# Performance work log

Hardware: AMD Instinct MI355X
Metric: run time of the kernel (lower is better)

## Reference

```python
import jax, jax.numpy as jnp
import numpy as np

L, B, D = 64, 2048, 512

def setup_inputs() -> dict:
    key = jax.random.key(0)
    ks = jax.random.split(key, 8)
    x = jax.random.normal(ks[0], (L, B, D), dtype=jnp.float32)
    # learned parameters (torch inits them to ones; random here for a nontrivial test)
    weight_x = 1.0 + 0.1 * jax.random.normal(ks[1], (L, D), dtype=jnp.float32)
    weight_g = 1.0 + 0.1 * jax.random.normal(ks[2], (L, D), dtype=jnp.float32)
    weight_h = 1.0 + 0.1 * jax.random.normal(ks[3], (L, D), dtype=jnp.float32)
    weight_u = 1.0 + 0.1 * jax.random.normal(ks[4], (L, D), dtype=jnp.float32)
    mask = jax.random.uniform(ks[5], (L, D), dtype=jnp.float32)
    fc_w = jax.random.normal(ks[6], (1, D), dtype=jnp.float32) / np.sqrt(D)
    fc_b = jax.random.normal(ks[7], (1,), dtype=jnp.float32) / np.sqrt(D)
    return {"x": x, "weight_x": weight_x, "weight_g": weight_g,
            "weight_h": weight_h, "weight_u": weight_u, "mask": mask,
            "fc_w": fc_w, "fc_b": fc_b}

def reference(x, weight_x, weight_g, weight_h, weight_u, mask, fc_w, fc_b):
    # x: [L, B, D]; per-step weights broadcast [D] over [B, D]
    xb0 = x[0]                               # x_bar[0] = x[0]
    h0 = jnp.tanh(x[0] * weight_x[0])        # h[0]
    xb1 = h0 * weight_g[0] + x[0]            # x_bar[1]

    def step(carry, inputs):
        h_prev, xbar_t = carry
        x_t, wx, wg, wh, wu, m = inputs
        x_trans = x_t * m + xbar_t * (1.0 - m)
        u = jnp.tanh(x_trans * wx)
        f = jax.nn.sigmoid(h_prev * wh + u * wu) * m
        h_t = f * h_prev + jnp.minimum(1.0 - f, u)
        h_t = h0 + jax.nn.relu(h_t - h0)
        xbar_next = h_t * wg + x_trans
        return (h_t, xbar_next), xbar_t

    _, xb_seq = jax.lax.scan(
        step, (h0, xb1),
        (x[1:], weight_x[1:], weight_g[1:], weight_h[1:], weight_u[1:], mask[1:]))
    # x_bar = [x_bar[0], x_bar[1], ..., x_bar[L-1]]  (x_bar[L] is never written in torch)
    x_bar = jnp.concatenate([xb0[None], xb_seq], axis=0)  # [L, B, D]
    pred = jax.nn.sigmoid(jnp.einsum('lbd,od->lbo', x_bar, fc_w) + fc_b)  # [L, B, 1]
    return pred
```

## Files before the change

### kernel.cpp

```cpp
#include <hip/hip_runtime.h>

typedef float f4 __attribute__((ext_vector_type(4)));
typedef float f2 __attribute__((ext_vector_type(2)));

#define LL 64
#define BB 2048
#define DD 512
#define GB 2
#define NBLK (BB / GB)
#define DEPTH 4

__device__ __forceinline__ float fexp2(float x){ return __builtin_amdgcn_exp2f(x); }
__device__ __forceinline__ float frcpf_(float x){ return __builtin_amdgcn_rcpf(x); }
__device__ __forceinline__ float fsigm(float z){ return frcpf_(1.0f + fexp2(-1.442695040888963f*z)); }
__device__ __forceinline__ float ftanh_(float z){ return 1.0f - 2.0f*frcpf_(1.0f + fexp2(2.885390081777927f*z)); }

__device__ __forceinline__ f4 ld4(const float* __restrict__ p){
  return *(const f4*)p;
}
__device__ __forceinline__ f4 vexp2(f4 v){
  f4 r; r[0]=fexp2(v[0]); r[1]=fexp2(v[1]); r[2]=fexp2(v[2]); r[3]=fexp2(v[3]); return r;
}
__device__ __forceinline__ f4 vrcp(f4 v){
  f4 r; r[0]=frcpf_(v[0]); r[1]=frcpf_(v[1]); r[2]=frcpf_(v[2]); r[3]=frcpf_(v[3]); return r;
}

__device__ __forceinline__ float quad_reduce_dpp(float v){
  int t1 = __builtin_amdgcn_update_dpp(0, __builtin_bit_cast(int, v),
                                       0xB1 , 0xF, 0xF, true);
  v += __builtin_bit_cast(float, t1);
  int t2 = __builtin_amdgcn_update_dpp(0, __builtin_bit_cast(int, v),
                                       0x4E , 0xF, 0xF, true);
  v += __builtin_bit_cast(float, t2);
  return v;
}

__global__ __launch_bounds__(128, 1) void rnn_fused_kernel(
    const float* __restrict__ x,
    const float* __restrict__ wxp, const float* __restrict__ wgp,
    const float* __restrict__ whp, const float* __restrict__ wup,
    const float* __restrict__ mp,  const float* __restrict__ fcw,
    const float* __restrict__ fcb, float* __restrict__ out)
{
  __shared__ float part[GB][LL][33];
  const int tid = threadIdx.x;
  const int b0  = blockIdx.x;
  const int d0  = tid << 2;
  const int grp = tid >> 2;

  const f4 fw = ld4(fcw + d0);
  const f2 fwlo = __builtin_shufflevector(fw, fw, 0, 1);
  const f2 fwhi = __builtin_shufflevector(fw, fw, 2, 3);
  const size_t PL = (size_t)BB * DD;

  const float* xbase[GB];
  #pragma unroll
  for (int g = 0; g < GB; ++g)
    xbase[g] = x + (size_t)(b0 * GB + g) * DD + d0;

  f4 xq[GB][DEPTH];
  f4 wxq[DEPTH], wgq[DEPTH], whq[DEPTH], wuq[DEPTH], mmq[DEPTH];
  #pragma unroll
  for (int k = 0; k < DEPTH; ++k){
    const int s = 1 + k;
    #pragma unroll
    for (int g = 0; g < GB; ++g)
      xq[g][k] = ld4(xbase[g] + (size_t)s * PL);
    wxq[k] = ld4(wxp + s * DD + d0);
    wgq[k] = ld4(wgp + s * DD + d0);
    whq[k] = ld4(whp + s * DD + d0);
    wuq[k] = ld4(wup + s * DD + d0);
    mmq[k] = ld4(mp  + s * DD + d0);
  }

  f4 w0x = ld4(wxp + d0);
  f4 w0g = ld4(wgp + d0);
  f4 h0v[GB], h[GB], xb[GB];
  #pragma unroll
  for (int g = 0; g < GB; ++g){
    f4 x0 = ld4(xbase[g]);
    float c0 = quad_reduce_dpp(x0[0]*fw[0] + x0[1]*fw[1] + x0[2]*fw[2] + x0[3]*fw[3]);
    if ((tid & 3) == 0) part[g][0][grp] = c0;

    float c1 = 0.0f;
    #pragma unroll
    for (int j = 0; j < 4; ++j){
      h0v[g][j] = ftanh_(x0[j] * w0x[j]);
      xb[g][j]  = h0v[g][j] * w0g[j] + x0[j];
      c1       += xb[g][j] * fw[j];
    }
    h[g] = h0v[g];
    c1 = quad_reduce_dpp(c1);
    if ((tid & 3) == 0) part[g][1][grp] = c1;
  }

  #pragma unroll 4
  for (int t = 1; t < LL - 1; ++t){
    const int tpn = (t + DEPTH <= LL - 2) ? (t + DEPTH) : (LL - 2);
    f4 xC[GB];
    #pragma unroll
    for (int g = 0; g < GB; ++g)
      xC[g] = ld4(xbase[g] + (size_t)tpn * PL);
    f4 wxn = ld4(wxp + tpn * DD + d0);
    f4 wgn = ld4(wgp + tpn * DD + d0);
    f4 whn = ld4(whp + tpn * DD + d0);
    f4 wun = ld4(wup + tpn * DD + d0);
    f4 mmn = ld4(mp  + tpn * DD + d0);

    f4 wxs = wxq[0] * 2.885390081777927f;
    f4 whs = whq[0] * -1.442695040888963f;
    f4 wus = wuq[0] * -1.442695040888963f;
    f4 wgc = wgq[0];
    f4 mmc = mmq[0];

    #pragma unroll
    for (int g = 0; g < GB; ++g){
      f4 xtr  = xb[g] + mmc * (xq[g][0] - xb[g]);
      f4 u    = 1.0f - 2.0f * vrcp(1.0f + vexp2(xtr * wxs));
      f4 sarg = h[g] * whs + u * wus;
      f4 ff   = vrcp(1.0f + vexp2(sarg)) * mmc;
      f4 mn   = __builtin_elementwise_min(1.0f - ff, u);
      f4 hn   = ff * h[g] + mn;
      hn      = __builtin_elementwise_max(hn, h0v[g]);
      h[g]  = hn;
      xb[g] = hn * wgc + xtr;

      f2 c2 = __builtin_shufflevector(xb[g], xb[g], 0, 1) * fwlo
            + __builtin_shufflevector(xb[g], xb[g], 2, 3) * fwhi;
      float cc = quad_reduce_dpp(c2[0] + c2[1]);
      if ((tid & 3) == 0) part[g][t + 1][grp] = cc;

      #pragma unroll
      for (int k = 0; k < DEPTH - 1; ++k) xq[g][k] = xq[g][k + 1];
      xq[g][DEPTH - 1] = xC[g];
    }

    #pragma unroll
    for (int k = 0; k < DEPTH - 1; ++k){
      wxq[k] = wxq[k + 1]; wgq[k] = wgq[k + 1]; whq[k] = whq[k + 1];
      wuq[k] = wuq[k + 1]; mmq[k] = mmq[k + 1];
    }
    wxq[DEPTH - 1] = wxn; wgq[DEPTH - 1] = wgn; whq[DEPTH - 1] = whn;
    wuq[DEPTH - 1] = wun; mmq[DEPTH - 1] = mmn;
  }

  __syncthreads();

  {
    const int l = tid & 63;
    const int g = tid >> 6;
    float s = 0.0f;
    #pragma unroll
    for (int j = 0; j < 32; ++j) s += part[g][l][j];
    out[(size_t)l * BB + (b0 * GB + g)] = fsigm(s + fcb[0]);
  }
}

extern "C" void kernel_launch(void* const* d_in, const int* in_sizes, int n_in,
                              void* d_out, int out_size, void* d_ws, size_t ws_size,
                              hipStream_t stream)
{
  const float* x   = (const float*)d_in[0];
  const float* wx  = (const float*)d_in[1];
  const float* wg  = (const float*)d_in[2];
  const float* wh  = (const float*)d_in[3];
  const float* wu  = (const float*)d_in[4];
  const float* m   = (const float*)d_in[5];
  const float* fcw = (const float*)d_in[6];
  const float* fcb = (const float*)d_in[7];
  float* out = (float*)d_out;
  rnn_fused_kernel<<<dim3(NBLK), dim3(128), 0, stream>>>(x, wx, wg, wh, wu, m, fcw, fcb, out);
}
```

Before: 52.40 us.

## Process one batch row per block with shallower prefetch and higher occupancy

Each block now handles a single batch row instead of two, so the grid doubles to 2048 blocks. Prefetch depth drops from 4 to 2 and launch bounds now ask for 4 blocks per CU, which cuts register pressure and lets more waves overlap the serial recurrence latency. The cost is shallower per-thread memory-level parallelism, the per-step weight loads are no longer shared across two rows, and half the threads sit idle in the final reduction.

```diff
diff --git a/kernel.cpp b/kernel.cpp
--- a/kernel.cpp
+++ b/kernel.cpp
@@ -6,9 +6,8 @@
 #define LL 64
 #define BB 2048
 #define DD 512
-#define GB 2
-#define NBLK (BB / GB)
-#define DEPTH 4
+#define NBLK BB
+#define DEPTH 2
 
 __device__ __forceinline__ float fexp2(float x){ return __builtin_amdgcn_exp2f(x); }
 __device__ __forceinline__ float frcpf_(float x){ return __builtin_amdgcn_rcpf(x); }
@@ -35,16 +34,16 @@
   return v;
 }
 
-__global__ __launch_bounds__(128, 1) void rnn_fused_kernel(
+__global__ __launch_bounds__(128, 4) void rnn_fused_kernel(
     const float* __restrict__ x,
     const float* __restrict__ wxp, const float* __restrict__ wgp,
     const float* __restrict__ whp, const float* __restrict__ wup,
     const float* __restrict__ mp,  const float* __restrict__ fcw,
     const float* __restrict__ fcb, float* __restrict__ out)
 {
-  __shared__ float part[GB][LL][33];
+  __shared__ float part[LL][33];
   const int tid = threadIdx.x;
-  const int b0  = blockIdx.x;
+  const int b   = blockIdx.x;
   const int d0  = tid << 2;
   const int grp = tid >> 2;
 
@@ -53,19 +52,14 @@
   const f2 fwhi = __builtin_shufflevector(fw, fw, 2, 3);
   const size_t PL = (size_t)BB * DD;
 
-  const float* xbase[GB];
-  #pragma unroll
-  for (int g = 0; g < GB; ++g)
-    xbase[g] = x + (size_t)(b0 * GB + g) * DD + d0;
+  const float* xbase = x + (size_t)b * DD + d0;
 
-  f4 xq[GB][DEPTH];
+  f4 xq[DEPTH];
   f4 wxq[DEPTH], wgq[DEPTH], whq[DEPTH], wuq[DEPTH], mmq[DEPTH];
   #pragma unroll
   for (int k = 0; k < DEPTH; ++k){
     const int s = 1 + k;
-    #pragma unroll
-    for (int g = 0; g < GB; ++g)
-      xq[g][k] = ld4(xbase[g] + (size_t)s * PL);
+    xq[k]  = ld4(xbase + (size_t)s * PL);
     wxq[k] = ld4(wxp + s * DD + d0);
     wgq[k] = ld4(wgp + s * DD + d0);
     whq[k] = ld4(whp + s * DD + d0);
@@ -75,32 +69,28 @@
 
   f4 w0x = ld4(wxp + d0);
   f4 w0g = ld4(wgp + d0);
-  f4 h0v[GB], h[GB], xb[GB];
-  #pragma unroll
-  for (int g = 0; g < GB; ++g){
-    f4 x0 = ld4(xbase[g]);
+  f4 h0v, h, xb;
+  {
+    f4 x0 = ld4(xbase);
     float c0 = quad_reduce_dpp(x0[0]*fw[0] + x0[1]*fw[1] + x0[2]*fw[2] + x0[3]*fw[3]);
-    if ((tid & 3) == 0) part[g][0][grp] = c0;
+    if ((tid & 3) == 0) part[0][grp] = c0;
 
     float c1 = 0.0f;
     #pragma unroll
     for (int j = 0; j < 4; ++j){
-      h0v[g][j] = ftanh_(x0[j] * w0x[j]);
-      xb[g][j]  = h0v[g][j] * w0g[j] + x0[j];
-      c1       += xb[g][j] * fw[j];
+      h0v[j] = ftanh_(x0[j] * w0x[j]);
+      xb[j]  = h0v[j] * w0g[j] + x0[j];
+      c1    += xb[j] * fw[j];
     }
-    h[g] = h0v[g];
+    h = h0v;
     c1 = quad_reduce_dpp(c1);
-    if ((tid & 3) == 0) part[g][1][grp] = c1;
+    if ((tid & 3) == 0) part[1][grp] = c1;
   }
 
-  #pragma unroll 4
+  #pragma unroll 2
   for (int t = 1; t < LL - 1; ++t){
     const int tpn = (t + DEPTH <= LL - 2) ? (t + DEPTH) : (LL - 2);
-    f4 xC[GB];
-    #pragma unroll
-    for (int g = 0; g < GB; ++g)
-      xC[g] = ld4(xbase[g] + (size_t)tpn * PL);
+    f4 xC  = ld4(xbase + (size_t)tpn * PL);
     f4 wxn = ld4(wxp + tpn * DD + d0);
     f4 wgn = ld4(wgp + tpn * DD + d0);
     f4 whn = ld4(whp + tpn * DD + d0);
@@ -113,46 +103,41 @@
     f4 wgc = wgq[0];
     f4 mmc = mmq[0];
 
-    #pragma unroll
-    for (int g = 0; g < GB; ++g){
-      f4 xtr  = xb[g] + mmc * (xq[g][0] - xb[g]);
+    {
+      f4 xtr  = xb + mmc * (xq[0] - xb);
       f4 u    = 1.0f - 2.0f * vrcp(1.0f + vexp2(xtr * wxs));
-      f4 sarg = h[g] * whs + u * wus;
+      f4 sarg = h * whs + u * wus;
       f4 ff   = vrcp(1.0f + vexp2(sarg)) * mmc;
       f4 mn   = __builtin_elementwise_min(1.0f - ff, u);
-      f4 hn   = ff * h[g] + mn;
-      hn      = __builtin_elementwise_max(hn, h0v[g]);
-      h[g]  = hn;
-      xb[g] = hn * wgc + xtr;
+      f4 hn   = ff * h + mn;
+      hn      = __builtin_elementwise_max(hn, h0v);
+      h  = hn;
+      xb = hn * wgc + xtr;
 
-      f2 c2 = __builtin_shufflevector(xb[g], xb[g], 0, 1) * fwlo
-            + __builtin_shufflevector(xb[g], xb[g], 2, 3) * fwhi;
+      f2 c2 = __builtin_shufflevector(xb, xb, 0, 1) * fwlo
+            + __builtin_shufflevector(xb, xb, 2, 3) * fwhi;
       float cc = quad_reduce_dpp(c2[0] + c2[1]);
-      if ((tid & 3) == 0) part[g][t + 1][grp] = cc;
-
-      #pragma unroll
-      for (int k = 0; k < DEPTH - 1; ++k) xq[g][k] = xq[g][k + 1];
-      xq[g][DEPTH - 1] = xC[g];
+      if ((tid & 3) == 0) part[t + 1][grp] = cc;
     }
 
     #pragma unroll
     for (int k = 0; k < DEPTH - 1; ++k){
+      xq[k] = xq[k + 1];
       wxq[k] = wxq[k + 1]; wgq[k] = wgq[k + 1]; whq[k] = whq[k + 1];
       wuq[k] = wuq[k + 1]; mmq[k] = mmq[k + 1];
     }
+    xq[DEPTH - 1] = xC;
     wxq[DEPTH - 1] = wxn; wgq[DEPTH - 1] = wgn; whq[DEPTH - 1] = whn;
     wuq[DEPTH - 1] = wun; mmq[DEPTH - 1] = mmn;
   }
 
   __syncthreads();
 
-  {
-    const int l = tid & 63;
-    const int g = tid >> 6;
+  if (tid < LL){
     float s = 0.0f;
     #pragma unroll
-    for (int j = 0; j < 32; ++j) s += part[g][l][j];
-    out[(size_t)l * BB + (b0 * GB + g)] = fsigm(s + fcb[0]);
+    for (int j = 0; j < 32; ++j) s += part[tid][j];
+    out[(size_t)tid * BB + b] = fsigm(s + fcb[0]);
   }
 }
 
```

New measurement: 69.66 us. 1.33x slower.
